# Kernel tuning notes

Measured on AMD Instinct MI355X. Metric: run time of the kernel, lower is better.

## Reference

```python
import jax, jax.numpy as jnp
import numpy as np

B, T, C, H, M, MEM_FREQ = 1, 2048, 768, 12, 64, 64


def setup_inputs() -> dict:
    key = jax.random.key(0)
    k1, k2, k3 = jax.random.split(key, 3)
    x = jax.random.normal(k1, (B, T, C), jnp.float32)
    # landmark ('mem') token every MEM_FREQ positions, as in landmark-attention data prep
    is_mem = jnp.broadcast_to((jnp.arange(T) % MEM_FREQ == MEM_FREQ - 1)[None, :], (B, T))
    w_qkv = 0.02 * jax.random.normal(k2, (C, 3 * C), jnp.float32)
    b_qkv = jnp.zeros((3 * C,), jnp.float32)
    w_proj = 0.02 * jax.random.normal(k3, (C, C), jnp.float32)
    b_proj = jnp.zeros((C,), jnp.float32)
    return {"x": x, "is_mem": is_mem, "w_qkv": w_qkv, "b_qkv": b_qkv,
            "w_proj": w_proj, "b_proj": b_proj}


def _grouped_softmax(att, im, mask, last_sec):
    """LandmarkGroupedSoftmaxFunction + landmark_grouped_softmax (eval, no dropout).
    att/im/mask/last_sec: (B,H,T,T); softmax over last dim grouped into M buckets."""
    neg = -jnp.inf
    last_and_rest = last_sec | mask
    full_access = im | last_and_rest
    mem_group_idx = jnp.cumsum(im.astype(jnp.int32), axis=-1)  # (B,H,T,T)
    resp = jnp.where(last_and_rest | im, M - 1, mem_group_idx)  # bucket id per key

    R = att.shape[0] * att.shape[1] * att.shape[2]
    Tk = att.shape[3]
    xf = att.reshape(R, Tk)
    idxf = resp.reshape(R, Tk)

    row_max = jax.vmap(lambda xr, ir: jnp.full((M,), neg, xr.dtype).at[ir].max(xr))
    row_sum = jax.vmap(lambda xr, ir: jnp.zeros((M,), xr.dtype).at[ir].add(xr))

    max_by_group = row_max(xf, idxf)                                   # (R,M)
    maxes = jnp.take_along_axis(max_by_group, idxf, axis=-1)
    safe_max = jnp.where(jnp.isinf(maxes), 0.0, maxes)
    x_exp = jnp.exp(xf - safe_max)
    denom_g = row_sum(x_exp, idxf)
    denom = jnp.take_along_axis(denom_g, idxf, axis=-1)
    small = denom < 0.5
    probs = jnp.where(small, 0.0, x_exp / jnp.where(small, 1.0, denom))

    imf = im.reshape(R, Tk)
    lsf = last_sec.reshape(R, Tk)
    faf = full_access.reshape(R, Tk)
    # group_prob[g] = prob of landmark g; last slot = mass of last (current) section
    gp_idx = jnp.where(imf, mem_group_idx.reshape(R, Tk) - 1, M - 1)
    group_prob = row_sum(jnp.where(imf, probs, 0.0), gp_idx)
    group_prob = group_prob.at[:, M - 1].set(jnp.sum(probs * lsf, axis=-1))
    gathered = jnp.take_along_axis(group_prob, idxf, axis=-1)
    mult = jnp.where(faf, lsf.astype(probs.dtype), gathered)
    return (probs * mult).reshape(att.shape)


def reference(x, is_mem, w_qkv, b_qkv, w_proj, b_proj):
    Bx, Tx, Cx = x.shape
    hd = Cx // H
    qkv = x @ w_qkv + b_qkv
    q, k, v = jnp.split(qkv, 3, axis=-1)
    q = q.reshape(Bx, Tx, H, hd).transpose(0, 2, 1, 3)  # (B,H,T,hd)
    k = k.reshape(Bx, Tx, H, hd).transpose(0, 2, 1, 3)
    v = v.reshape(Bx, Tx, H, hd).transpose(0, 2, 1, 3)

    att = jnp.einsum('bhqd,bhkd->bhqk', q, k) * (1.0 / np.sqrt(hd))
    causal = jnp.triu(jnp.ones((Tx, Tx), bool), 1)[None, None]  # True = masked
    att = jnp.where(causal, -jnp.inf, att)

    im = jnp.broadcast_to(is_mem[:, None, None, :], (Bx, H, Tx, Tx))
    im_i = im.astype(jnp.int32)
    mem_ids = jnp.where(causal, 0, jnp.cumsum(im_i, axis=-1) - im_i)
    last_sec = mem_ids == jnp.max(mem_ids, axis=-1, keepdims=True)
    mask = causal | (im & last_sec)   # landmarks of the current section are masked
    last_sec = last_sec & ~mask
    im = im & ~mask
    att = jnp.where(mask, -jnp.inf, att)

    probs = _grouped_softmax(att, im, mask, last_sec)
    y = jnp.einsum('bhqk,bhkd->bhqd', probs, v)
    y = y.transpose(0, 2, 1, 3).reshape(Bx, Tx, Cx)
    return y @ w_proj + b_proj
```

## Files before the change

kernel.cpp:

```cpp
#include <hip/hip_runtime.h>
#include <hip/hip_bf16.h>
#include <math.h>

#define TT 2048
#define CC 768
#define NH 12
#define HDIM 64
#define QKVLD 2304
#define NSEC 32
#define NCHMAX 8

typedef short bf16x8 __attribute__((ext_vector_type(8)));
typedef float f32x4 __attribute__((ext_vector_type(4)));

#define MFMA16(a, b, c) __builtin_amdgcn_mfma_f32_16x16x32_bf16(a, b, c, 0, 0, 0)

__device__ __forceinline__ ushort f2bf(float f) {
  __hip_bfloat16 h = __float2bfloat16(f);
  return *reinterpret_cast<ushort*>(&h);
}

__device__ __forceinline__ float bf2f(ushort u) {
  __hip_bfloat16 b = *reinterpret_cast<__hip_bfloat16*>(&u);
  return __bfloat162float(b);
}

__device__ __forceinline__ void gload_lds16(const ushort* g, ushort* l) {
  __builtin_amdgcn_global_load_lds(
      (const __attribute__((address_space(1))) void*)g,
      (__attribute__((address_space(3))) void*)l, 16, 0, 0);
}

__device__ __forceinline__ int chunk_base(int q) {
  const int a = q >> 2, b = q & 3;
  return q + 2 * a * (a - 1) + a * b;
}

__global__ __launch_bounds__(256) void convert_bf16_kernel(
    const float* __restrict__ in, ushort* __restrict__ out, int n) {
  int i = (blockIdx.x * 256 + threadIdx.x) * 8;
  if (i >= n) return;
  float4 a = *(const float4*)&in[i];
  float4 b = *(const float4*)&in[i + 4];
  bf16x8 o;
  o[0] = (short)f2bf(a.x); o[1] = (short)f2bf(a.y);
  o[2] = (short)f2bf(a.z); o[3] = (short)f2bf(a.w);
  o[4] = (short)f2bf(b.x); o[5] = (short)f2bf(b.y);
  o[6] = (short)f2bf(b.z); o[7] = (short)f2bf(b.w);
  *(bf16x8*)&out[i] = o;
}

__global__ __launch_bounds__(256) void transpose2_kernel(
    const float* __restrict__ w_qkv, const float* __restrict__ w_proj,
    ushort* __restrict__ wqkvT, ushort* __restrict__ wprojT) {
  const int z = blockIdx.z;
  const float* in = z ? w_proj : w_qkv;
  ushort* out = z ? wprojT : wqkvT;
  const int N = z ? CC : QKVLD;
  const int K = CC;
  if (blockIdx.x * 64 >= N) return;

  __shared__ float tile[64][65];
  const int t = threadIdx.x;
  const int kb = blockIdx.y * 64, nb = blockIdx.x * 64;
  const int rg = t >> 4, cg = t & 15;
#pragma unroll
  for (int r = 0; r < 4; ++r) {
    float4 v = *(const float4*)&in[(size_t)(kb + rg * 4 + r) * N + nb + cg * 4];
    tile[rg * 4 + r][cg * 4 + 0] = v.x;
    tile[rg * 4 + r][cg * 4 + 1] = v.y;
    tile[rg * 4 + r][cg * 4 + 2] = v.z;
    tile[rg * 4 + r][cg * 4 + 3] = v.w;
  }
  __syncthreads();
#pragma unroll
  for (int r = 0; r < 4; ++r) {
    const int nl = rg * 4 + r;
    ushort4 o;
    o.x = f2bf(tile[cg * 4 + 0][nl]);
    o.y = f2bf(tile[cg * 4 + 1][nl]);
    o.z = f2bf(tile[cg * 4 + 2][nl]);
    o.w = f2bf(tile[cg * 4 + 3][nl]);
    *(ushort4*)&out[(size_t)(nb + nl) * K + kb + cg * 4] = o;
  }
}

__global__ __launch_bounds__(256) void gemm_bt_bf16_kernel(
    const ushort* __restrict__ A, const ushort* __restrict__ Bt,
    const float* __restrict__ bias,
    ushort* __restrict__ qkvb, ushort* __restrict__ vT,
    float* __restrict__ Cf,
    int M, int N, int K) {
  __shared__ ushort As[64 * 64];
  __shared__ ushort Bs[64 * 64];
  const int tid = threadIdx.x;
  const int wid = tid >> 6, lane = tid & 63;
  const int lr = lane & 15, lg = lane >> 4;
  const int wr = wid >> 1, wc = wid & 1;
  const int bm = blockIdx.y * 64, bn = blockIdx.x * 64;

  f32x4 acc[2][2];
#pragma unroll
  for (int m = 0; m < 2; ++m)
#pragma unroll
    for (int n = 0; n < 2; ++n) acc[m][n] = (f32x4){0.f, 0.f, 0.f, 0.f};

  const int srow7 = lane >> 3;
  const int scolw = ((lane & 7) ^ srow7) * 8;
  const int rswz = lr & 7;

  for (int k0 = 0; k0 < K; k0 += 64) {
    __syncthreads();
#pragma unroll
    for (int half = 0; half < 2; ++half) {
      const int row = half * 32 + wid * 8 + srow7;
      gload_lds16(A  + (size_t)(bm + row) * K + k0 + scolw,
                  &As[(half * 32 + wid * 8) * 64]);
      gload_lds16(Bt + (size_t)(bn + row) * K + k0 + scolw,
                  &Bs[(half * 32 + wid * 8) * 64]);
    }
    __syncthreads();
#pragma unroll
    for (int kk = 0; kk < 2; ++kk) {
      bf16x8 af[2], bfr[2];
#pragma unroll
      for (int m = 0; m < 2; ++m)
        af[m] = *(const bf16x8*)
            &As[(wr * 32 + m * 16 + lr) * 64 + (((kk * 4 + lg) ^ rswz) * 8)];
#pragma unroll
      for (int n = 0; n < 2; ++n)
        bfr[n] = *(const bf16x8*)
            &Bs[(wc * 32 + n * 16 + lr) * 64 + (((kk * 4 + lg) ^ rswz) * 8)];
#pragma unroll
      for (int m = 0; m < 2; ++m)
#pragma unroll
        for (int n = 0; n < 2; ++n)
          acc[m][n] = MFMA16(af[m], bfr[n], acc[m][n]);
    }
  }

  float bb[2];
#pragma unroll
  for (int n = 0; n < 2; ++n) bb[n] = bias[bn + wc * 32 + n * 16 + lr];

  if (Cf) {
#pragma unroll
    for (int m = 0; m < 2; ++m)
#pragma unroll
      for (int n = 0; n < 2; ++n)
#pragma unroll
        for (int r = 0; r < 4; ++r) {
          const int row = bm + wr * 32 + m * 16 + lg * 4 + r;
          const int col = bn + wc * 32 + n * 16 + lr;
          Cf[(size_t)row * N + col] = acc[m][n][r] + bb[n];
        }
  } else if (bn < 768) {
#pragma unroll
    for (int m = 0; m < 2; ++m)
#pragma unroll
      for (int n = 0; n < 2; ++n)
#pragma unroll
        for (int r = 0; r < 4; ++r) {
          const int row = bm + wr * 32 + m * 16 + lg * 4 + r;
          const int col = bn + wc * 32 + n * 16 + lr;
          qkvb[(size_t)row * QKVLD + col] = f2bf((acc[m][n][r] + bb[n]) * 0.125f);
        }
  } else if (bn < 1536) {
#pragma unroll
    for (int m = 0; m < 2; ++m)
#pragma unroll
      for (int n = 0; n < 2; ++n)
#pragma unroll
        for (int r = 0; r < 4; ++r) {
          const int row = bm + wr * 32 + m * 16 + lg * 4 + r;
          const int col = bn + wc * 32 + n * 16 + lr;
          qkvb[(size_t)row * QKVLD + col] = f2bf(acc[m][n][r] + bb[n]);
        }
  } else {
#pragma unroll
    for (int m = 0; m < 2; ++m)
#pragma unroll
      for (int n = 0; n < 2; ++n) {
        const int row0 = bm + wr * 32 + m * 16 + lg * 4;
        const int vrow = bn + wc * 32 + n * 16 + lr - 1536;
        ushort4 o;
        o.x = f2bf(acc[m][n][0] + bb[n]);
        o.y = f2bf(acc[m][n][1] + bb[n]);
        o.z = f2bf(acc[m][n][2] + bb[n]);
        o.w = f2bf(acc[m][n][3] + bb[n]);
        *(ushort4*)&vT[(size_t)vrow * TT + row0] = o;
      }
  }
}

__global__ __launch_bounds__(256, 8) void attn_chunk_kernel(
    const ushort* __restrict__ qkvb,
    const ushort* __restrict__ vT,
    ushort* __restrict__ pacc,
    float* __restrict__ pstats) {
  const int c = blockIdx.x, qsec = blockIdx.y, h = blockIdx.z;
  if (c * 4 > qsec) return;
  const int tid = threadIdx.x;
  const int wid = tid >> 6, lane = tid & 63;
  const int lr = lane & 15, lg = lane >> 4;

  __shared__ ushort Kl[64 * 64];
  __shared__ ushort Vl[64 * 64];
  __shared__ ushort Pl[4 * 16 * 64];

  const int qloc = wid * 16 + lr;
  const ushort* qp = qkvb + (size_t)(qsec * 64 + qloc) * QKVLD + h * HDIM + lg * 8;
  const bf16x8 qf0 = *(const bf16x8*)qp;
  const bf16x8 qf1 = *(const bf16x8*)(qp + 32);

  f32x4 accy[4];
#pragma unroll
  for (int nt = 0; nt < 4; ++nt) accy[nt] = (f32x4){0.f, 0.f, 0.f, 0.f};
  float mrun = -INFINITY, dl = 0.f;

  const int s0 = c * 4;
  const int send = (s0 + 3 < qsec) ? s0 + 3 : qsec;

  const int srow = wid * 8 + (lane >> 3);
  const int scolw = ((lane & 7) ^ (lane >> 3)) * 8;
  const ushort* ksrc = qkvb + (size_t)(s0 * 64 + srow) * QKVLD + CC + h * HDIM + scolw;
  const ushort* vsrc = vT + (size_t)(h * HDIM + srow) * TT + s0 * 64 + scolw;
  ushort* kdst = &Kl[wid * 512];
  ushort* vdst = &Vl[wid * 512];
  const int rswz = lr & 7;

  for (int s = s0; s <= send; ++s) {
    __syncthreads();
    gload_lds16(ksrc,                          kdst);
    gload_lds16(ksrc + (size_t)32 * QKVLD,     kdst + 2048);
    gload_lds16(vsrc,                          vdst);
    gload_lds16(vsrc + (size_t)32 * TT,        vdst + 2048);
    ksrc += (size_t)64 * QKVLD;
    vsrc += 64;
    __syncthreads();

    f32x4 sacc[4];
#pragma unroll
    for (int nt = 0; nt < 4; ++nt) sacc[nt] = (f32x4){0.f, 0.f, 0.f, 0.f};
#pragma unroll
    for (int nt = 0; nt < 4; ++nt) {
      bf16x8 kf0 = *(const bf16x8*)&Kl[(nt * 16 + lr) * 64 + ((lg ^ rswz) * 8)];
      bf16x8 kf1 = *(const bf16x8*)&Kl[(nt * 16 + lr) * 64 + (((4 + lg) ^ rswz) * 8)];
      sacc[nt] = MFMA16(kf0, qf0, sacc[nt]);
      sacc[nt] = MFMA16(kf1, qf1, sacc[nt]);
    }

    const bool curq = (s == qsec);
    float lmv = 0.f;
    if (!curq) {
      lmv = __shfl(sacc[3][3], 48 + lr);
      if (lg == 3) sacc[3][3] = -INFINITY;
    } else {
      const int lim = qloc < 62 ? qloc : 62;
#pragma unroll
      for (int nt = 0; nt < 4; ++nt)
#pragma unroll
        for (int r = 0; r < 4; ++r)
          if (nt * 16 + lg * 4 + r > lim) sacc[nt][r] = -INFINITY;
    }

    float vmax = sacc[0][0];
#pragma unroll
    for (int nt = 0; nt < 4; ++nt)
#pragma unroll
      for (int r = 0; r < 4; ++r) vmax = fmaxf(vmax, sacc[nt][r]);
    vmax = fmaxf(vmax, __shfl_xor(vmax, 16));
    vmax = fmaxf(vmax, __shfl_xor(vmax, 32));

    float base_;
    if (curq) {
      float mn = fmaxf(mrun, vmax);
      float sc = __expf(mrun - mn);
#pragma unroll
      for (int nt = 0; nt < 4; ++nt) accy[nt] *= sc;
      dl *= sc; mrun = mn; base_ = mn;
    } else {
      base_ = vmax;
    }

    float ssum = 0.f;
#pragma unroll
    for (int nt = 0; nt < 4; ++nt)
#pragma unroll
      for (int r = 0; r < 4; ++r) {
        sacc[nt][r] = __expf(sacc[nt][r] - base_);
        ssum += sacc[nt][r];
      }
    ssum += __shfl_xor(ssum, 16);
    ssum += __shfl_xor(ssum, 32);

    float coef;
    if (!curq) {
      float mn = fmaxf(mrun, lmv);
      float sc = __expf(mrun - mn);
      float el = __expf(lmv - mn);
#pragma unroll
      for (int nt = 0; nt < 4; ++nt) accy[nt] *= sc;
      dl = dl * sc + el; mrun = mn;
      coef = el / ssum;
    } else {
      coef = 1.f;
      dl += ssum;
    }

    {
      ushort* prow = &Pl[wid * 1024 + lr * 64];
#pragma unroll
      for (int nt = 0; nt < 4; ++nt) {
        ushort4 o;
        o.x = f2bf(sacc[nt][0] * coef);
        o.y = f2bf(sacc[nt][1] * coef);
        o.z = f2bf(sacc[nt][2] * coef);
        o.w = f2bf(sacc[nt][3] * coef);
        *(ushort4*)&prow[(((nt * 2 + (lg >> 1)) ^ rswz) * 8) + (lg & 1) * 4] = o;
      }

      bf16x8 pf0 = *(const bf16x8*)&prow[(lg ^ rswz) * 8];
      bf16x8 pf1 = *(const bf16x8*)&prow[((4 + lg) ^ rswz) * 8];
#pragma unroll
      for (int nt = 0; nt < 4; ++nt) {
        bf16x8 vf0 = *(const bf16x8*)&Vl[(nt * 16 + lr) * 64 + ((lg ^ rswz) * 8)];
        bf16x8 vf1 = *(const bf16x8*)&Vl[(nt * 16 + lr) * 64 + (((4 + lg) ^ rswz) * 8)];
        accy[nt] = MFMA16(vf0, pf0, accy[nt]);
        accy[nt] = MFMA16(vf1, pf1, accy[nt]);
      }
    }
  }

  const int slot = (chunk_base(qsec) + c) * NH + h;
  ushort* ap = pacc + (size_t)slot * 4096;
#pragma unroll
  for (int nt = 0; nt < 4; ++nt)
#pragma unroll
    for (int r = 0; r < 4; ++r)
      ap[(nt * 16 + lg * 4 + r) * 64 + wid * 16 + lr] = f2bf(accy[nt][r]);
  if (lg == 0) {
    float* st = pstats + (size_t)slot * 128;
    st[(wid * 16 + lr) * 2 + 0] = mrun;
    st[(wid * 16 + lr) * 2 + 1] = dl;
  }
}

__global__ __launch_bounds__(256) void attn_merge_kernel(
    const ushort* __restrict__ pacc, const float* __restrict__ pstats,
    ushort* __restrict__ y) {
  const int qsec = blockIdx.x, h = blockIdx.y;
  const int tid = threadIdx.x;
  const int w = tid >> 6, q = tid & 63;
  const int nch = (qsec >> 2) + 1;
  const int sbase = chunk_base(qsec);
  __shared__ float Lt[64][65];

  float M = -INFINITY;
  for (int cc = 0; cc < nch; ++cc)
    M = fmaxf(M, pstats[(size_t)((sbase + cc) * NH + h) * 128 + q * 2]);
  float D = 0.f;
  for (int cc = 0; cc < nch; ++cc) {
    const float* st = pstats + (size_t)((sbase + cc) * NH + h) * 128 + q * 2;
    D += __expf(st[0] - M) * st[1];
  }
  const float invD = 1.f / D;

  float val[16];
#pragma unroll
  for (int j = 0; j < 16; ++j) val[j] = 0.f;
  for (int cc = 0; cc < nch; ++cc) {
    const int slot = (sbase + cc) * NH + h;
    const float cw = __expf(pstats[(size_t)slot * 128 + q * 2] - M) * invD;
    const ushort* ap = pacc + (size_t)slot * 4096 + w * 16 * 64 + q;
#pragma unroll
    for (int j = 0; j < 16; ++j) val[j] += cw * bf2f(ap[j * 64]);
  }
#pragma unroll
  for (int j = 0; j < 16; ++j) Lt[w * 16 + j][q] = val[j];
  __syncthreads();

  const int d = tid & 63;
#pragma unroll
  for (int j = 0; j < 16; ++j) {
    const int qq = w * 16 + j;
    y[(size_t)(qsec * 64 + qq) * CC + h * HDIM + d] = f2bf(Lt[d][qq]);
  }
}

extern "C" void kernel_launch(void* const* d_in, const int* in_sizes, int n_in,
                              void* d_out, int out_size, void* d_ws, size_t ws_size,
                              hipStream_t stream) {
  const float* x      = (const float*)d_in[0];
  const float* w_qkv  = (const float*)d_in[2];
  const float* b_qkv  = (const float*)d_in[3];
  const float* w_proj = (const float*)d_in[4];
  const float* b_proj = (const float*)d_in[5];
  float* out = (float*)d_out;

  ushort* wprojT = (ushort*)d_ws;
  ushort* qkvb   = wprojT + (size_t)CC * CC;
  ushort* vT     = qkvb + (size_t)TT * QKVLD;
  ushort* y      = vT + (size_t)CC * TT;
  ushort* pacc   = y + (size_t)TT * CC;
  float*  pstats = (float*)(pacc + (size_t)1728 * 4096);
  ushort* xb     = pacc;
  ushort* wqkvT  = xb + (size_t)TT * CC;

  convert_bf16_kernel<<<TT * CC / (256 * 8), 256, 0, stream>>>(x, xb, TT * CC);
  transpose2_kernel<<<dim3(QKVLD / 64, CC / 64, 2), 256, 0, stream>>>(
      w_qkv, w_proj, wqkvT, wprojT);

  gemm_bt_bf16_kernel<<<dim3(QKVLD / 64, TT / 64), 256, 0, stream>>>(
      xb, wqkvT, b_qkv, qkvb, vT, nullptr, TT, QKVLD, CC);

  attn_chunk_kernel<<<dim3(NCHMAX, NSEC, NH), 256, 0, stream>>>(
      qkvb, vT, pacc, pstats);
  attn_merge_kernel<<<dim3(NSEC, NH), 256, 0, stream>>>(pacc, pstats, y);

  gemm_bt_bf16_kernel<<<dim3(CC / 64, TT / 64), 256, 0, stream>>>(
      y, wprojT, b_proj, nullptr, nullptr, out, TT, CC, CC);
}
```

Baseline: 79.81 us.

## Double-buffer LDS tiles in GEMM and attention, merge prep kernels

The GEMM and attention-chunk kernels now use two LDS buffers each. The next K/V or A/B tile is fetched with global_load_lds while the current tile is being computed, which removes one barrier per iteration and hides load latency. The bf16 conversion of x and the two weight transposes are merged into a single prep launch to save one kernel launch. The extra LDS buffers raise shared memory use per block, which can reduce occupancy in the attention kernel.

```diff
diff --git a/kernel.cpp b/kernel.cpp
--- a/kernel.cpp
+++ b/kernel.cpp
@@ -36,33 +36,37 @@
   return q + 2 * a * (a - 1) + a * b;
 }
 
-__global__ __launch_bounds__(256) void convert_bf16_kernel(
-    const float* __restrict__ in, ushort* __restrict__ out, int n) {
-  int i = (blockIdx.x * 256 + threadIdx.x) * 8;
-  if (i >= n) return;
-  float4 a = *(const float4*)&in[i];
-  float4 b = *(const float4*)&in[i + 4];
-  bf16x8 o;
-  o[0] = (short)f2bf(a.x); o[1] = (short)f2bf(a.y);
-  o[2] = (short)f2bf(a.z); o[3] = (short)f2bf(a.w);
-  o[4] = (short)f2bf(b.x); o[5] = (short)f2bf(b.y);
-  o[6] = (short)f2bf(b.z); o[7] = (short)f2bf(b.w);
-  *(bf16x8*)&out[i] = o;
-}
-
-__global__ __launch_bounds__(256) void transpose2_kernel(
-    const float* __restrict__ w_qkv, const float* __restrict__ w_proj,
-    ushort* __restrict__ wqkvT, ushort* __restrict__ wprojT) {
-  const int z = blockIdx.z;
-  const float* in = z ? w_proj : w_qkv;
-  ushort* out = z ? wprojT : wqkvT;
-  const int N = z ? CC : QKVLD;
+__global__ __launch_bounds__(256) void prep_kernel(
+    const float* __restrict__ x, const float* __restrict__ w_qkv,
+    const float* __restrict__ w_proj,
+    ushort* __restrict__ xb, ushort* __restrict__ wqkvT,
+    ushort* __restrict__ wprojT) {
+  const int bid = blockIdx.x;
+  const int t = threadIdx.x;
+  __shared__ float tile[64][65];
+
+  if (bid < 768) {
+    const int i = (bid * 256 + t) * 8;
+    float4 a = *(const float4*)&x[i];
+    float4 b = *(const float4*)&x[i + 4];
+    bf16x8 o;
+    o[0] = (short)f2bf(a.x); o[1] = (short)f2bf(a.y);
+    o[2] = (short)f2bf(a.z); o[3] = (short)f2bf(a.w);
+    o[4] = (short)f2bf(b.x); o[5] = (short)f2bf(b.y);
+    o[6] = (short)f2bf(b.z); o[7] = (short)f2bf(b.w);
+    *(bf16x8*)&xb[i] = o;
+    return;
+  }
+
+  const bool qkv = bid < 1200;
+  const int tb = qkv ? bid - 768 : bid - 1200;
+  const float* in = qkv ? w_qkv : w_proj;
+  ushort* out = qkv ? wqkvT : wprojT;
+  const int N = qkv ? QKVLD : CC;
+  const int ntx = N / 64;
+  const int nb = (tb % ntx) * 64, kb = (tb / ntx) * 64;
   const int K = CC;
-  if (blockIdx.x * 64 >= N) return;
-
-  __shared__ float tile[64][65];
-  const int t = threadIdx.x;
-  const int kb = blockIdx.y * 64, nb = blockIdx.x * 64;
+
   const int rg = t >> 4, cg = t & 15;
 #pragma unroll
   for (int r = 0; r < 4; ++r) {
@@ -91,8 +95,8 @@
     ushort* __restrict__ qkvb, ushort* __restrict__ vT,
     float* __restrict__ Cf,
     int M, int N, int K) {
-  __shared__ ushort As[64 * 64];
-  __shared__ ushort Bs[64 * 64];
+  __shared__ ushort As[2][64 * 64];
+  __shared__ ushort Bs[2][64 * 64];
   const int tid = threadIdx.x;
   const int wid = tid >> 6, lane = tid & 63;
   const int lr = lane & 15, lg = lane >> 4;
@@ -109,34 +113,45 @@
   const int scolw = ((lane & 7) ^ srow7) * 8;
   const int rswz = lr & 7;
 
+#pragma unroll
+  for (int half = 0; half < 2; ++half) {
+    const int row = half * 32 + wid * 8 + srow7;
+    gload_lds16(A  + (size_t)(bm + row) * K + scolw, &As[0][(half * 32 + wid * 8) * 64]);
+    gload_lds16(Bt + (size_t)(bn + row) * K + scolw, &Bs[0][(half * 32 + wid * 8) * 64]);
+  }
+  int cur = 0;
+
   for (int k0 = 0; k0 < K; k0 += 64) {
     __syncthreads();
-#pragma unroll
-    for (int half = 0; half < 2; ++half) {
-      const int row = half * 32 + wid * 8 + srow7;
-      gload_lds16(A  + (size_t)(bm + row) * K + k0 + scolw,
-                  &As[(half * 32 + wid * 8) * 64]);
-      gload_lds16(Bt + (size_t)(bn + row) * K + k0 + scolw,
-                  &Bs[(half * 32 + wid * 8) * 64]);
-    }
-    __syncthreads();
+    if (k0 + 64 < K) {
+      const int nb_ = cur ^ 1;
+#pragma unroll
+      for (int half = 0; half < 2; ++half) {
+        const int row = half * 32 + wid * 8 + srow7;
+        gload_lds16(A  + (size_t)(bm + row) * K + k0 + 64 + scolw,
+                    &As[nb_][(half * 32 + wid * 8) * 64]);
+        gload_lds16(Bt + (size_t)(bn + row) * K + k0 + 64 + scolw,
+                    &Bs[nb_][(half * 32 + wid * 8) * 64]);
+      }
+    }
 #pragma unroll
     for (int kk = 0; kk < 2; ++kk) {
       bf16x8 af[2], bfr[2];
 #pragma unroll
       for (int m = 0; m < 2; ++m)
         af[m] = *(const bf16x8*)
-            &As[(wr * 32 + m * 16 + lr) * 64 + (((kk * 4 + lg) ^ rswz) * 8)];
+            &As[cur][(wr * 32 + m * 16 + lr) * 64 + (((kk * 4 + lg) ^ rswz) * 8)];
 #pragma unroll
       for (int n = 0; n < 2; ++n)
         bfr[n] = *(const bf16x8*)
-            &Bs[(wc * 32 + n * 16 + lr) * 64 + (((kk * 4 + lg) ^ rswz) * 8)];
+            &Bs[cur][(wc * 32 + n * 16 + lr) * 64 + (((kk * 4 + lg) ^ rswz) * 8)];
 #pragma unroll
       for (int m = 0; m < 2; ++m)
 #pragma unroll
         for (int n = 0; n < 2; ++n)
           acc[m][n] = MFMA16(af[m], bfr[n], acc[m][n]);
     }
+    cur ^= 1;
   }
 
   float bb[2];
@@ -204,8 +219,8 @@
   const int wid = tid >> 6, lane = tid & 63;
   const int lr = lane & 15, lg = lane >> 4;
 
-  __shared__ ushort Kl[64 * 64];
-  __shared__ ushort Vl[64 * 64];
+  __shared__ ushort Kl[2][64 * 64];
+  __shared__ ushort Vl[2][64 * 64];
   __shared__ ushort Pl[4 * 16 * 64];
 
   const int qloc = wid * 16 + lr;
@@ -225,27 +240,33 @@
   const int scolw = ((lane & 7) ^ (lane >> 3)) * 8;
   const ushort* ksrc = qkvb + (size_t)(s0 * 64 + srow) * QKVLD + CC + h * HDIM + scolw;
   const ushort* vsrc = vT + (size_t)(h * HDIM + srow) * TT + s0 * 64 + scolw;
-  ushort* kdst = &Kl[wid * 512];
-  ushort* vdst = &Vl[wid * 512];
   const int rswz = lr & 7;
+
+  gload_lds16(ksrc,                      &Kl[0][wid * 512]);
+  gload_lds16(ksrc + (size_t)32 * QKVLD, &Kl[0][wid * 512 + 2048]);
+  gload_lds16(vsrc,                      &Vl[0][wid * 512]);
+  gload_lds16(vsrc + (size_t)32 * TT,    &Vl[0][wid * 512 + 2048]);
+  int cur = 0;
 
   for (int s = s0; s <= send; ++s) {
     __syncthreads();
-    gload_lds16(ksrc,                          kdst);
-    gload_lds16(ksrc + (size_t)32 * QKVLD,     kdst + 2048);
-    gload_lds16(vsrc,                          vdst);
-    gload_lds16(vsrc + (size_t)32 * TT,        vdst + 2048);
-    ksrc += (size_t)64 * QKVLD;
-    vsrc += 64;
-    __syncthreads();
+    if (s < send) {
+      ksrc += (size_t)64 * QKVLD;
+      vsrc += 64;
+      const int nb_ = cur ^ 1;
+      gload_lds16(ksrc,                      &Kl[nb_][wid * 512]);
+      gload_lds16(ksrc + (size_t)32 * QKVLD, &Kl[nb_][wid * 512 + 2048]);
+      gload_lds16(vsrc,                      &Vl[nb_][wid * 512]);
+      gload_lds16(vsrc + (size_t)32 * TT,    &Vl[nb_][wid * 512 + 2048]);
+    }
 
     f32x4 sacc[4];
 #pragma unroll
     for (int nt = 0; nt < 4; ++nt) sacc[nt] = (f32x4){0.f, 0.f, 0.f, 0.f};
 #pragma unroll
     for (int nt = 0; nt < 4; ++nt) {
-      bf16x8 kf0 = *(const bf16x8*)&Kl[(nt * 16 + lr) * 64 + ((lg ^ rswz) * 8)];
-      bf16x8 kf1 = *(const bf16x8*)&Kl[(nt * 16 + lr) * 64 + (((4 + lg) ^ rswz) * 8)];
+      bf16x8 kf0 = *(const bf16x8*)&Kl[cur][(nt * 16 + lr) * 64 + ((lg ^ rswz) * 8)];
+      bf16x8 kf1 = *(const bf16x8*)&Kl[cur][(nt * 16 + lr) * 64 + (((4 + lg) ^ rswz) * 8)];
       sacc[nt] = MFMA16(kf0, qf0, sacc[nt]);
       sacc[nt] = MFMA16(kf1, qf1, sacc[nt]);
     }
@@ -324,12 +345,13 @@
       bf16x8 pf1 = *(const bf16x8*)&prow[((4 + lg) ^ rswz) * 8];
 #pragma unroll
       for (int nt = 0; nt < 4; ++nt) {
-        bf16x8 vf0 = *(const bf16x8*)&Vl[(nt * 16 + lr) * 64 + ((lg ^ rswz) * 8)];
-        bf16x8 vf1 = *(const bf16x8*)&Vl[(nt * 16 + lr) * 64 + (((4 + lg) ^ rswz) * 8)];
+        bf16x8 vf0 = *(const bf16x8*)&Vl[cur][(nt * 16 + lr) * 64 + ((lg ^ rswz) * 8)];
+        bf16x8 vf1 = *(const bf16x8*)&Vl[cur][(nt * 16 + lr) * 64 + (((4 + lg) ^ rswz) * 8)];
         accy[nt] = MFMA16(vf0, pf0, accy[nt]);
         accy[nt] = MFMA16(vf1, pf1, accy[nt]);
       }
     }
+    cur ^= 1;
   }
 
   const int slot = (chunk_base(qsec) + c) * NH + h;
@@ -407,9 +429,7 @@
   ushort* xb     = pacc;
   ushort* wqkvT  = xb + (size_t)TT * CC;
 
-  convert_bf16_kernel<<<TT * CC / (256 * 8), 256, 0, stream>>>(x, xb, TT * CC);
-  transpose2_kernel<<<dim3(QKVLD / 64, CC / 64, 2), 256, 0, stream>>>(
-      w_qkv, w_proj, wqkvT, wprojT);
+  prep_kernel<<<1344, 256, 0, stream>>>(x, w_qkv, w_proj, xb, wqkvT, wprojT);
 
   gemm_bt_bf16_kernel<<<dim3(QKVLD / 64, TT / 64), 256, 0, stream>>>(
       xb, wqkvT, b_qkv, qkvb, vT, nullptr, TT, QKVLD, CC);
```

After: 79.12 us. Within noise of the previous version (-0.9%).
